# Kernel tuning notes

Measured on AMD Instinct MI355X. Metric: run time of the kernel, lower is better.

The kernel has to match this reference:

```python
import jax, jax.numpy as jnp
import numpy as np

B, N_SOURCES, H, W = 32, 262144, 256, 256


def setup_inputs() -> dict:
    key = jax.random.key(0)
    k1, k2, k3, k4 = jax.random.split(key, 4)
    return {
        "point_rates": jax.random.uniform(k1, (B, N_SOURCES), dtype=jnp.float32),
        "spatial": jax.random.uniform(k2, (B, 2, H, W), dtype=jnp.float32),
        "gia": jax.random.uniform(k3, (B, H, W), dtype=jnp.float32),
        "all_source_coords": jax.random.uniform(k4, (N_SOURCES, 2), dtype=jnp.float32),
    }


def reference(point_rates, spatial, gia, all_source_coords):
    # point_rates: [B, N], spatial: [B, 2, H, W], gia: [B, H, W], coords: [N, 2]
    _, _, h, w = spatial.shape
    sx = all_source_coords[:, 0]  # [N]
    sy = all_source_coords[:, 1]  # [N]

    def per_batch(pr, sp, g):
        # pr: [N], sp: [2, H, W], g: [H, W]
        xmin, xmax = sp[0].min(), sp[0].max()
        ymin, ymax = sp[1].min(), sp[1].max()
        in_view = ((sx >= xmin) & (sx <= xmax) & (sy >= ymin) & (sy <= ymax))
        nx = (sx - xmin) / (xmax - xmin)
        ny = (sy - ymin) / (ymax - ymin)
        px = jnp.clip(jnp.round(nx * (w - 1)).astype(jnp.int32), 0, w - 1)
        py = jnp.clip(jnp.round(ny * (h - 1)).astype(jnp.int32), 0, h - 1)
        # out-of-view sources contribute zero (instead of being gathered out)
        em = pr * g[py, px] * in_view.astype(pr.dtype)  # [N]
        field = jnp.zeros((h, w), dtype=pr.dtype).at[py, px].add(em)
        return field[None]  # [1, H, W]

    return jax.vmap(per_batch)(point_rates, spatial, gia)  # [B, 1, H, W]
```

## Files before the change

kernel.cpp:

```cpp
#include <hip/hip_runtime.h>
#include <math.h>

#define BATCH 32
#define NSRC  262144
#define HH    256
#define WW    256
#define HW    (HH * WW)
#define NBLK  16

#define ZBANDS 16
#define ZBAND_PIX (HW / ZBANDS)
#define ZCAP   18432
#define SPILL_CAP 131072
#define FIX_SCALE 524288.0f
#define FIX_INV   (1.0f / 524288.0f)
#define WS_ZCURS_OFF  8192
#define WS_ZSPCNT_OFF 10240
#define WS_ZSPILL_OFF 16384
#define WS_ZARENA_OFF (WS_ZSPILL_OFF + SPILL_CAP * 8)
#define WS_Z_BYTES    (WS_ZARENA_OFF + (size_t)BATCH * ZBANDS * ZCAP * 4)

#define FB_BANDS 8
#define FB_BAND_PIX (HW / FB_BANDS)

__global__ void box_kernel(const float* __restrict__ spatial,
                           float4* __restrict__ partials,
                           unsigned int* __restrict__ zero_tab,
                           int zero_n) {
    const int b   = blockIdx.y;
    const int blk = blockIdx.x;
    const int tid = threadIdx.x;

    if (zero_tab && blk == 0 && b == 0) {
        for (int j = tid; j < zero_n; j += 256) zero_tab[j] = 0u;
    }

    const int chunk = HW / NBLK;
    const float* xs = spatial + (size_t)b * 2 * HW + (size_t)blk * chunk;
    const float* ys = xs + HW;

    float xmn = 1e30f, xmx = -1e30f, ymn = 1e30f, ymx = -1e30f;
    const float4* xs4 = (const float4*)xs;
    const float4* ys4 = (const float4*)ys;
#pragma unroll
    for (int k = 0; k < 4; k++) {
        float4 vx = xs4[k * 256 + tid];
        float4 vy = ys4[k * 256 + tid];
        xmn = fminf(xmn, fminf(fminf(vx.x, vx.y), fminf(vx.z, vx.w)));
        xmx = fmaxf(xmx, fmaxf(fmaxf(vx.x, vx.y), fmaxf(vx.z, vx.w)));
        ymn = fminf(ymn, fminf(fminf(vy.x, vy.y), fminf(vy.z, vy.w)));
        ymx = fmaxf(ymx, fmaxf(fmaxf(vy.x, vy.y), fmaxf(vy.z, vy.w)));
    }
#pragma unroll
    for (int off = 32; off > 0; off >>= 1) {
        xmn = fminf(xmn, __shfl_down(xmn, off));
        xmx = fmaxf(xmx, __shfl_down(xmx, off));
        ymn = fminf(ymn, __shfl_down(ymn, off));
        ymx = fmaxf(ymx, __shfl_down(ymx, off));
    }
    __shared__ float4 s[4];
    if ((tid & 63) == 0) s[tid >> 6] = make_float4(xmn, xmx, ymn, ymx);
    __syncthreads();
    if (tid == 0) {
        float4 r = s[0];
#pragma unroll
        for (int wv = 1; wv < 4; wv++) {
            float4 t = s[wv];
            r.x = fminf(r.x, t.x); r.y = fmaxf(r.y, t.y);
            r.z = fminf(r.z, t.z); r.w = fmaxf(r.w, t.w);
        }
        partials[b * NBLK + blk] = r;
    }
}

__device__ __forceinline__ float4 fold_box(const float4* __restrict__ partials,
                                           int b, int tid, float4* sbox) {
    if (tid < 64) {
        float4 p = make_float4(1e30f, -1e30f, 1e30f, -1e30f);
        if (tid < NBLK) p = partials[b * NBLK + tid];
        float xmn = p.x, xmx = p.y, ymn = p.z, ymx = p.w;
#pragma unroll
        for (int off = 8; off > 0; off >>= 1) {
            xmn = fminf(xmn, __shfl_down(xmn, off));
            xmx = fmaxf(xmx, __shfl_down(xmx, off));
            ymn = fminf(ymn, __shfl_down(ymn, off));
            ymx = fmaxf(ymx, __shfl_down(ymx, off));
        }
        if (tid == 0) *sbox = make_float4(xmn, xmx, ymn, ymx);
    }
    __syncthreads();
    return *sbox;
}

__device__ __forceinline__ int route_of(float cx, float cy, float xmin,
                                        float ymin, float invx, float invy) {
    const float nx = __fmul_rn(__fsub_rn(cx, xmin), invx);
    const float ny = __fmul_rn(__fsub_rn(cy, ymin), invy);
    int px = (int)rintf(__fmul_rn(nx, 255.0f));
    int py = (int)rintf(__fmul_rn(ny, 255.0f));
    px = px < 0 ? 0 : (px > 255 ? 255 : px);
    py = py < 0 ? 0 : (py > 255 ? 255 : py);
    return py * WW + px;
}


__global__ __launch_bounds__(256) void scatter_ballot_kernel(
    const float* __restrict__ point_rates, const float2* __restrict__ coords,
    const float4* __restrict__ partials, unsigned int* __restrict__ cursors,
    unsigned int* __restrict__ arena, unsigned int* __restrict__ spill_cnt,
    uint2* __restrict__ spill) {
    const int b    = blockIdx.y;
    const int tid  = threadIdx.x;
    const int wave = tid >> 6;
    const int lane = tid & 63;
    __shared__ float4 sbox;
    __shared__ unsigned int wtot[4][ZBANDS];
    __shared__ unsigned int wbase[4][ZBANDS];

    const float4 box = fold_box(partials, b, tid, &sbox);
    const float xmin = box.x, xmax = box.y, ymin = box.z, ymax = box.w;
    const float invx = __fdiv_rn(1.0f, __fsub_rn(xmax, xmin));
    const float invy = __fdiv_rn(1.0f, __fsub_rn(ymax, ymin));

    const unsigned long long below =
        (lane == 63) ? 0x7FFFFFFFFFFFFFFFull : ((1ull << lane) - 1ull);

    const float* prb = point_rates + (size_t)b * NSRC;
    const int base = blockIdx.x * 4096;

    unsigned int cur_slice = 0u;

    unsigned int ent[16];
    unsigned int meta[16];

#pragma unroll
    for (int k = 0; k < 16; k++) {
        const int i = base + k * 256 + tid;
        const float2 c = coords[i];
        const float  pr = prb[i];
        const bool valid =
            !(c.x < xmin || c.x > xmax || c.y < ymin || c.y > ymax);
        const int idx = route_of(c.x, c.y, xmin, ymin, invx, invy);
        const int z = valid ? (idx >> 12) : ZBANDS;
        const unsigned int fixed =
            (unsigned int)(__fmul_rn(pr, FIX_SCALE) + 0.5f);
        ent[k] = (unsigned int)(idx & (ZBAND_PIX - 1)) | (fixed << 12);

        const unsigned long long bv = __ballot(valid);
        const unsigned long long b0 = __ballot((z & 1) != 0);
        const unsigned long long b1 = __ballot((z & 2) != 0);
        const unsigned long long b2 = __ballot((z & 4) != 0);
        const unsigned long long b3 = __ballot((z & 8) != 0);
        unsigned long long m = bv;
        m &= (lane & 1) ? b0 : ~b0;
        m &= (lane & 2) ? b1 : ~b1;
        m &= (lane & 4) ? b2 : ~b2;
        m &= (lane & 8) ? b3 : ~b3;
        const unsigned int cnt = (unsigned int)__popcll(m);
        const unsigned int curbase = __shfl(cur_slice, z);
        const unsigned long long mown = __shfl(m, z);
        const unsigned int rank = (unsigned int)__popcll(mown & below);
        meta[k] = valid ? (((unsigned int)z << 16) | (curbase + rank))
                        : 0xFFFFFFFFu;
        cur_slice += cnt;
    }

    if (lane < ZBANDS) wtot[wave][lane] = cur_slice;
    __syncthreads();

    if (wave == 0 && lane < ZBANDS) {
        unsigned int t0 = wtot[0][lane], t1 = wtot[1][lane],
                     t2 = wtot[2][lane], t3 = wtot[3][lane];
        unsigned int tot = t0 + t1 + t2 + t3;
        unsigned int g = atomicAdd(&cursors[b * ZBANDS + lane], tot);
        wbase[0][lane] = g;
        wbase[1][lane] = g + t0;
        wbase[2][lane] = g + t0 + t1;
        wbase[3][lane] = g + t0 + t1 + t2;
    }
    __syncthreads();

#pragma unroll
    for (int k = 0; k < 16; k++) {
        const unsigned int mt = meta[k];
        if (mt == 0xFFFFFFFFu) continue;
        const unsigned int z = mt >> 16;
        const unsigned int slot = wbase[wave][z] + (mt & 0xFFFFu);
        if (slot < ZCAP) {
            arena[((size_t)b * ZBANDS + z) * ZCAP + slot] = ent[k];
        } else {
            const unsigned int pos = atomicAdd(spill_cnt, 1u);
            if (pos < SPILL_CAP) {
                const unsigned int pix =
                    (z << 12) | (ent[k] & (ZBAND_PIX - 1));
                const int i = base + k * 256 + tid;
                spill[pos] = make_uint2(((unsigned int)b << 16) | pix,
                                        __float_as_uint(prb[i]));
            }
        }
    }
}

__global__ __launch_bounds__(1024) void accum_g_kernel(
    const unsigned int* __restrict__ arena, const float* __restrict__ gia,
    const unsigned int* __restrict__ cursors, float* __restrict__ out) {
    __shared__ unsigned int acc[ZBAND_PIX];
    const int z   = blockIdx.x;
    const int b   = blockIdx.y;
    const int tid = threadIdx.x;

    const unsigned int n_raw = cursors[b * ZBANDS + z];
    const float4* g4 =
        (const float4*)(gia + (size_t)b * HW + (size_t)z * ZBAND_PIX);
    float4 g = g4[tid];
    asm volatile("" : "+v"(g.x), "+v"(g.y), "+v"(g.z), "+v"(g.w));

    ((uint4*)acc)[tid] = make_uint4(0u, 0u, 0u, 0u);
    __syncthreads();

    unsigned int n = n_raw;
    if (n > ZCAP) n = ZCAP;
    const uint4* a4 = (const uint4*)(arena + ((size_t)b * ZBANDS + z) * ZCAP);

#define DO_E(w)                                                              \
    atomicAdd(&acc[(w) & (ZBAND_PIX - 1)], (w) >> 12);
    const unsigned int n4 = n >> 2;
    unsigned int j = tid;
    for (; j + 3u * 1024u < n4; j += 4u * 1024u) {
        uint4 e0 = a4[j];
        uint4 e1 = a4[j + 1024u];
        uint4 e2 = a4[j + 2048u];
        uint4 e3 = a4[j + 3072u];
        asm volatile(""
                     : "+v"(e0.x), "+v"(e0.y), "+v"(e0.z), "+v"(e0.w),
                       "+v"(e1.x), "+v"(e1.y), "+v"(e1.z), "+v"(e1.w),
                       "+v"(e2.x), "+v"(e2.y), "+v"(e2.z), "+v"(e2.w),
                       "+v"(e3.x), "+v"(e3.y), "+v"(e3.z), "+v"(e3.w));
        DO_E(e0.x) DO_E(e0.y) DO_E(e0.z) DO_E(e0.w)
        DO_E(e1.x) DO_E(e1.y) DO_E(e1.z) DO_E(e1.w)
        DO_E(e2.x) DO_E(e2.y) DO_E(e2.z) DO_E(e2.w)
        DO_E(e3.x) DO_E(e3.y) DO_E(e3.z) DO_E(e3.w)
    }
    for (; j < n4; j += 1024u) {
        const uint4 e = a4[j];
        DO_E(e.x) DO_E(e.y) DO_E(e.z) DO_E(e.w)
    }
    const unsigned int* a1 = (const unsigned int*)a4;
    for (unsigned int jj = (n4 << 2) + tid; jj < n; jj += 1024u) {
        const unsigned int w = a1[jj];
        DO_E(w)
    }
#undef DO_E
    __syncthreads();

    float4* o4 = (float4*)(out + (size_t)b * HW + (size_t)z * ZBAND_PIX);
    const uint4 a = ((const uint4*)acc)[tid];
    o4[tid] = make_float4(
        __fmul_rn(__fmul_rn((float)a.x, FIX_INV), g.x),
        __fmul_rn(__fmul_rn((float)a.y, FIX_INV), g.y),
        __fmul_rn(__fmul_rn((float)a.z, FIX_INV), g.z),
        __fmul_rn(__fmul_rn((float)a.w, FIX_INV), g.w));
}

__global__ void spill_kernel(const unsigned int* __restrict__ spill_cnt,
                             const uint2* __restrict__ spill,
                             const float* __restrict__ gia,
                             float* __restrict__ out) {
    unsigned int n = *spill_cnt;
    if (n > SPILL_CAP) n = SPILL_CAP;
    for (unsigned int j = blockIdx.x * 256 + threadIdx.x; j < n;
         j += gridDim.x * 256) {
        const uint2 e = spill[j];
        const unsigned int b = e.x >> 16;
        const unsigned int pix = e.x & 0xFFFFu;
        const float pr = __uint_as_float(e.y);
        atomicAdd(&out[(size_t)b * HW + pix],
                  __fmul_rn(pr, gia[(size_t)b * HW + pix]));
    }
}


__global__ __launch_bounds__(512) void accum_recompute_kernel(
    const float* __restrict__ point_rates, const float* __restrict__ gia,
    const float2* __restrict__ coords, const float4* __restrict__ partials,
    float* __restrict__ out) {
    __shared__ float acc[FB_BAND_PIX];
    __shared__ float4 sbox;
    const int z   = blockIdx.x;
    const int b   = blockIdx.y;
    const int tid = threadIdx.x;

    const float4 box = fold_box(partials, b, tid, &sbox);
    const float xmin = box.x, xmax = box.y, ymin = box.z, ymax = box.w;
    const float invx = __fdiv_rn(1.0f, __fsub_rn(xmax, xmin));
    const float invy = __fdiv_rn(1.0f, __fsub_rn(ymax, ymin));

    for (int j = tid; j < FB_BAND_PIX; j += 512) acc[j] = 0.f;
    __syncthreads();

    const float* prb = point_rates + (size_t)b * NSRC;
    const float* gb  = gia + (size_t)b * HW;
    const int lo = z * FB_BAND_PIX, hi = lo + FB_BAND_PIX;

    for (int i = tid; i < NSRC; i += 512) {
        const float2 c = coords[i];
        if (c.x < xmin || c.x > xmax || c.y < ymin || c.y > ymax) continue;
        const int idx = route_of(c.x, c.y, xmin, ymin, invx, invy);
        if (idx < lo || idx >= hi) continue;
        const float em = __fmul_rn(prb[i], gb[idx]);
        atomicAdd(&acc[idx - lo], em);
    }
    __syncthreads();

    float4* o4 = (float4*)(out + (size_t)b * HW + (size_t)z * FB_BAND_PIX);
    const float4* a4 = (const float4*)acc;
    for (int j = tid; j < FB_BAND_PIX / 4; j += 512) o4[j] = a4[j];
}

extern "C" void kernel_launch(void* const* d_in, const int* in_sizes, int n_in,
                              void* d_out, int out_size, void* d_ws, size_t ws_size,
                              hipStream_t stream) {
    const float* point_rates = (const float*)d_in[0];
    const float* spatial     = (const float*)d_in[1];
    const float* gia         = (const float*)d_in[2];
    const float2* coords     = (const float2*)d_in[3];
    float* out = (float*)d_out;

    char* ws = (char*)d_ws;
    float4* partials = (float4*)ws;

    if (ws_size >= WS_Z_BYTES) {
        unsigned int* cursors   = (unsigned int*)(ws + WS_ZCURS_OFF);
        unsigned int* spill_cnt = (unsigned int*)(ws + WS_ZSPCNT_OFF);
        uint2*        spill     = (uint2*)(ws + WS_ZSPILL_OFF);
        unsigned int* arena     = (unsigned int*)(ws + WS_ZARENA_OFF);

        box_kernel<<<dim3(NBLK, BATCH), 256, 0, stream>>>(
            spatial, partials, cursors, BATCH * ZBANDS + 1);
        scatter_ballot_kernel<<<dim3(NSRC / 4096, BATCH), 256, 0, stream>>>(
            point_rates, coords, partials, cursors, arena, spill_cnt, spill);
        accum_g_kernel<<<dim3(ZBANDS, BATCH), 1024, 0, stream>>>(
            arena, gia, cursors, out);
        spill_kernel<<<4, 256, 0, stream>>>(spill_cnt, spill, gia, out);
    } else {
        box_kernel<<<dim3(NBLK, BATCH), 256, 0, stream>>>(
            spatial, partials, nullptr, 0);
        accum_recompute_kernel<<<dim3(FB_BANDS, BATCH), 512, 0, stream>>>(
            point_rates, gia, coords, partials, out);
    }
}
```

Baseline: 126.0 us.

## Stage binned scatter entries in LDS to coalesce arena writes

Instead of each thread writing its entries straight to scattered global arena slots, the block first sorts its entries by band into shared memory using a prefix scan of per-band totals. It then writes each band's run contiguously to the arena, so global stores are coalesced. The cost is extra LDS traffic, an additional barrier and 16KB more shared memory per block, which may lower occupancy. The spill path now rebuilds the rate from the fixed-point entry rather than reloading it, which changes the spilled value's precision.

```diff
diff --git a/kernel.cpp b/kernel.cpp
--- a/kernel.cpp
+++ b/kernel.cpp
@@ -116,6 +116,9 @@
     __shared__ float4 sbox;
     __shared__ unsigned int wtot[4][ZBANDS];
     __shared__ unsigned int wbase[4][ZBANDS];
+    __shared__ unsigned int boff[ZBANDS + 1];
+    __shared__ unsigned int gbase[ZBANDS];
+    __shared__ unsigned int sort_lds[4096];
 
     const float4 box = fold_box(partials, b, tid, &sbox);
     const float xmin = box.x, xmax = box.y, ymin = box.z, ymax = box.w;
@@ -169,14 +172,22 @@
     __syncthreads();
 
     if (wave == 0 && lane < ZBANDS) {
-        unsigned int t0 = wtot[0][lane], t1 = wtot[1][lane],
-                     t2 = wtot[2][lane], t3 = wtot[3][lane];
-        unsigned int tot = t0 + t1 + t2 + t3;
-        unsigned int g = atomicAdd(&cursors[b * ZBANDS + lane], tot);
-        wbase[0][lane] = g;
-        wbase[1][lane] = g + t0;
-        wbase[2][lane] = g + t0 + t1;
-        wbase[3][lane] = g + t0 + t1 + t2;
+        const unsigned int t0 = wtot[0][lane], t1 = wtot[1][lane],
+                           t2 = wtot[2][lane], t3 = wtot[3][lane];
+        const unsigned int tot = t0 + t1 + t2 + t3;
+        wbase[0][lane] = 0u;
+        wbase[1][lane] = t0;
+        wbase[2][lane] = t0 + t1;
+        wbase[3][lane] = t0 + t1 + t2;
+        unsigned int p = tot;
+#pragma unroll
+        for (int off = 1; off < ZBANDS; off <<= 1) {
+            const unsigned int t = __shfl_up(p, off);
+            if (lane >= off) p += t;
+        }
+        boff[lane] = p - tot;
+        if (lane == ZBANDS - 1) boff[ZBANDS] = p;
+        gbase[lane] = atomicAdd(&cursors[b * ZBANDS + lane], tot);
     }
     __syncthreads();
 
@@ -185,17 +196,30 @@
         const unsigned int mt = meta[k];
         if (mt == 0xFFFFFFFFu) continue;
         const unsigned int z = mt >> 16;
-        const unsigned int slot = wbase[wave][z] + (mt & 0xFFFFu);
-        if (slot < ZCAP) {
-            arena[((size_t)b * ZBANDS + z) * ZCAP + slot] = ent[k];
-        } else {
-            const unsigned int pos = atomicAdd(spill_cnt, 1u);
-            if (pos < SPILL_CAP) {
-                const unsigned int pix =
-                    (z << 12) | (ent[k] & (ZBAND_PIX - 1));
-                const int i = base + k * 256 + tid;
-                spill[pos] = make_uint2(((unsigned int)b << 16) | pix,
-                                        __float_as_uint(prb[i]));
+        sort_lds[boff[z] + wbase[wave][z] + (mt & 0xFFFFu)] = ent[k];
+    }
+    __syncthreads();
+
+    unsigned int* ab = arena + (size_t)b * ZBANDS * ZCAP;
+    for (int z = 0; z < ZBANDS; z++) {
+        const unsigned int lo = boff[z];
+        const unsigned int cnt = boff[z + 1] - lo;
+        const unsigned int g = gbase[z];
+        unsigned int* dst = ab + (size_t)z * ZCAP;
+        for (unsigned int j = tid; j < cnt; j += 256) {
+            const unsigned int e = sort_lds[lo + j];
+            const unsigned int slot = g + j;
+            if (slot < ZCAP) {
+                dst[slot] = e;
+            } else {
+                const unsigned int pos = atomicAdd(spill_cnt, 1u);
+                if (pos < SPILL_CAP) {
+                    const unsigned int pix =
+                        ((unsigned int)z << 12) | (e & (ZBAND_PIX - 1));
+                    const float pr = __fmul_rn((float)(e >> 12), FIX_INV);
+                    spill[pos] = make_uint2(((unsigned int)b << 16) | pix,
+                                            __float_as_uint(pr));
+                }
             }
         }
     }
```

Result: slower. 130.2 us (+3.3%).

## Replace band binning and LDS accumulation with direct global fixed-point atomics

Applied to the files above, without the earlier changes.

Drops the ballot-based band partitioning into an arena, the per-band shared-memory accumulation kernel, and the spill kernel. Each source now does a single global integer atomicAdd into a per-batch fixed-point accumulator, which is zeroed in box_kernel, and a simple elementwise finalize kernel multiplies by gia. This removes the arena write and read traffic and one kernel launch. In exchange it relies on many scattered global atomics, about 8M across 2M pixels, served by the L2.

```diff
diff --git a/kernel.cpp b/kernel.cpp
--- a/kernel.cpp
+++ b/kernel.cpp
@@ -8,31 +8,26 @@
 #define HW    (HH * WW)
 #define NBLK  16
 
-#define ZBANDS 16
-#define ZBAND_PIX (HW / ZBANDS)
-#define ZCAP   18432
-#define SPILL_CAP 131072
 #define FIX_SCALE 524288.0f
 #define FIX_INV   (1.0f / 524288.0f)
-#define WS_ZCURS_OFF  8192
-#define WS_ZSPCNT_OFF 10240
-#define WS_ZSPILL_OFF 16384
-#define WS_ZARENA_OFF (WS_ZSPILL_OFF + SPILL_CAP * 8)
-#define WS_Z_BYTES    (WS_ZARENA_OFF + (size_t)BATCH * ZBANDS * ZCAP * 4)
+#define WS_GACC_OFF   16384
+#define WS_FUSED_BYTES (WS_GACC_OFF + (size_t)BATCH * HW * 4)
 
 #define FB_BANDS 8
 #define FB_BAND_PIX (HW / FB_BANDS)
 
 __global__ void box_kernel(const float* __restrict__ spatial,
                            float4* __restrict__ partials,
-                           unsigned int* __restrict__ zero_tab,
-                           int zero_n) {
+                           unsigned int* __restrict__ gacc_zero) {
     const int b   = blockIdx.y;
     const int blk = blockIdx.x;
     const int tid = threadIdx.x;
 
-    if (zero_tab && blk == 0 && b == 0) {
-        for (int j = tid; j < zero_n; j += 256) zero_tab[j] = 0u;
+    if (gacc_zero) {
+        uint4* gz = (uint4*)(gacc_zero + ((size_t)b * NBLK + blk) * (HW / NBLK));
+#pragma unroll
+        for (int j = 0; j < HW / NBLK / 4 / 256; j++)
+            gz[j * 256 + tid] = make_uint4(0u, 0u, 0u, 0u);
     }
 
     const int chunk = HW / NBLK;
@@ -103,35 +98,21 @@
     return py * WW + px;
 }
 
-
-__global__ __launch_bounds__(256) void scatter_ballot_kernel(
+__global__ __launch_bounds__(256) void scatter_atomic_kernel(
     const float* __restrict__ point_rates, const float2* __restrict__ coords,
-    const float4* __restrict__ partials, unsigned int* __restrict__ cursors,
-    unsigned int* __restrict__ arena, unsigned int* __restrict__ spill_cnt,
-    uint2* __restrict__ spill) {
-    const int b    = blockIdx.y;
-    const int tid  = threadIdx.x;
-    const int wave = tid >> 6;
-    const int lane = tid & 63;
+    const float4* __restrict__ partials, unsigned int* __restrict__ gacc) {
+    const int b   = blockIdx.y;
+    const int tid = threadIdx.x;
     __shared__ float4 sbox;
-    __shared__ unsigned int wtot[4][ZBANDS];
-    __shared__ unsigned int wbase[4][ZBANDS];
 
     const float4 box = fold_box(partials, b, tid, &sbox);
     const float xmin = box.x, xmax = box.y, ymin = box.z, ymax = box.w;
     const float invx = __fdiv_rn(1.0f, __fsub_rn(xmax, xmin));
     const float invy = __fdiv_rn(1.0f, __fsub_rn(ymax, ymin));
 
-    const unsigned long long below =
-        (lane == 63) ? 0x7FFFFFFFFFFFFFFFull : ((1ull << lane) - 1ull);
-
     const float* prb = point_rates + (size_t)b * NSRC;
+    unsigned int* acc_b = gacc + (size_t)b * HW;
     const int base = blockIdx.x * 4096;
-
-    unsigned int cur_slice = 0u;
-
-    unsigned int ent[16];
-    unsigned int meta[16];
 
 #pragma unroll
     for (int k = 0; k < 16; k++) {
@@ -141,142 +122,23 @@
         const bool valid =
             !(c.x < xmin || c.x > xmax || c.y < ymin || c.y > ymax);
         const int idx = route_of(c.x, c.y, xmin, ymin, invx, invy);
-        const int z = valid ? (idx >> 12) : ZBANDS;
         const unsigned int fixed =
             (unsigned int)(__fmul_rn(pr, FIX_SCALE) + 0.5f);
-        ent[k] = (unsigned int)(idx & (ZBAND_PIX - 1)) | (fixed << 12);
-
-        const unsigned long long bv = __ballot(valid);
-        const unsigned long long b0 = __ballot((z & 1) != 0);
-        const unsigned long long b1 = __ballot((z & 2) != 0);
-        const unsigned long long b2 = __ballot((z & 4) != 0);
-        const unsigned long long b3 = __ballot((z & 8) != 0);
-        unsigned long long m = bv;
-        m &= (lane & 1) ? b0 : ~b0;
-        m &= (lane & 2) ? b1 : ~b1;
-        m &= (lane & 4) ? b2 : ~b2;
-        m &= (lane & 8) ? b3 : ~b3;
-        const unsigned int cnt = (unsigned int)__popcll(m);
-        const unsigned int curbase = __shfl(cur_slice, z);
-        const unsigned long long mown = __shfl(m, z);
-        const unsigned int rank = (unsigned int)__popcll(mown & below);
-        meta[k] = valid ? (((unsigned int)z << 16) | (curbase + rank))
-                        : 0xFFFFFFFFu;
-        cur_slice += cnt;
-    }
-
-    if (lane < ZBANDS) wtot[wave][lane] = cur_slice;
-    __syncthreads();
-
-    if (wave == 0 && lane < ZBANDS) {
-        unsigned int t0 = wtot[0][lane], t1 = wtot[1][lane],
-                     t2 = wtot[2][lane], t3 = wtot[3][lane];
-        unsigned int tot = t0 + t1 + t2 + t3;
-        unsigned int g = atomicAdd(&cursors[b * ZBANDS + lane], tot);
-        wbase[0][lane] = g;
-        wbase[1][lane] = g + t0;
-        wbase[2][lane] = g + t0 + t1;
-        wbase[3][lane] = g + t0 + t1 + t2;
-    }
-    __syncthreads();
-
-#pragma unroll
-    for (int k = 0; k < 16; k++) {
-        const unsigned int mt = meta[k];
-        if (mt == 0xFFFFFFFFu) continue;
-        const unsigned int z = mt >> 16;
-        const unsigned int slot = wbase[wave][z] + (mt & 0xFFFFu);
-        if (slot < ZCAP) {
-            arena[((size_t)b * ZBANDS + z) * ZCAP + slot] = ent[k];
-        } else {
-            const unsigned int pos = atomicAdd(spill_cnt, 1u);
-            if (pos < SPILL_CAP) {
-                const unsigned int pix =
-                    (z << 12) | (ent[k] & (ZBAND_PIX - 1));
-                const int i = base + k * 256 + tid;
-                spill[pos] = make_uint2(((unsigned int)b << 16) | pix,
-                                        __float_as_uint(prb[i]));
-            }
-        }
-    }
-}
-
-__global__ __launch_bounds__(1024) void accum_g_kernel(
-    const unsigned int* __restrict__ arena, const float* __restrict__ gia,
-    const unsigned int* __restrict__ cursors, float* __restrict__ out) {
-    __shared__ unsigned int acc[ZBAND_PIX];
-    const int z   = blockIdx.x;
-    const int b   = blockIdx.y;
-    const int tid = threadIdx.x;
-
-    const unsigned int n_raw = cursors[b * ZBANDS + z];
-    const float4* g4 =
-        (const float4*)(gia + (size_t)b * HW + (size_t)z * ZBAND_PIX);
-    float4 g = g4[tid];
-    asm volatile("" : "+v"(g.x), "+v"(g.y), "+v"(g.z), "+v"(g.w));
-
-    ((uint4*)acc)[tid] = make_uint4(0u, 0u, 0u, 0u);
-    __syncthreads();
-
-    unsigned int n = n_raw;
-    if (n > ZCAP) n = ZCAP;
-    const uint4* a4 = (const uint4*)(arena + ((size_t)b * ZBANDS + z) * ZCAP);
-
-#define DO_E(w)                                                              \
-    atomicAdd(&acc[(w) & (ZBAND_PIX - 1)], (w) >> 12);
-    const unsigned int n4 = n >> 2;
-    unsigned int j = tid;
-    for (; j + 3u * 1024u < n4; j += 4u * 1024u) {
-        uint4 e0 = a4[j];
-        uint4 e1 = a4[j + 1024u];
-        uint4 e2 = a4[j + 2048u];
-        uint4 e3 = a4[j + 3072u];
-        asm volatile(""
-                     : "+v"(e0.x), "+v"(e0.y), "+v"(e0.z), "+v"(e0.w),
-                       "+v"(e1.x), "+v"(e1.y), "+v"(e1.z), "+v"(e1.w),
-                       "+v"(e2.x), "+v"(e2.y), "+v"(e2.z), "+v"(e2.w),
-                       "+v"(e3.x), "+v"(e3.y), "+v"(e3.z), "+v"(e3.w));
-        DO_E(e0.x) DO_E(e0.y) DO_E(e0.z) DO_E(e0.w)
-        DO_E(e1.x) DO_E(e1.y) DO_E(e1.z) DO_E(e1.w)
-        DO_E(e2.x) DO_E(e2.y) DO_E(e2.z) DO_E(e2.w)
-        DO_E(e3.x) DO_E(e3.y) DO_E(e3.z) DO_E(e3.w)
-    }
-    for (; j < n4; j += 1024u) {
-        const uint4 e = a4[j];
-        DO_E(e.x) DO_E(e.y) DO_E(e.z) DO_E(e.w)
-    }
-    const unsigned int* a1 = (const unsigned int*)a4;
-    for (unsigned int jj = (n4 << 2) + tid; jj < n; jj += 1024u) {
-        const unsigned int w = a1[jj];
-        DO_E(w)
-    }
-#undef DO_E
-    __syncthreads();
-
-    float4* o4 = (float4*)(out + (size_t)b * HW + (size_t)z * ZBAND_PIX);
-    const uint4 a = ((const uint4*)acc)[tid];
-    o4[tid] = make_float4(
+        if (valid) atomicAdd(&acc_b[idx], fixed);
+    }
+}
+
+__global__ __launch_bounds__(256) void finalize_kernel(
+    const unsigned int* __restrict__ gacc, const float* __restrict__ gia,
+    float* __restrict__ out) {
+    const int gid = blockIdx.x * 256 + threadIdx.x;
+    const uint4  a = ((const uint4*)gacc)[gid];
+    const float4 g = ((const float4*)gia)[gid];
+    ((float4*)out)[gid] = make_float4(
         __fmul_rn(__fmul_rn((float)a.x, FIX_INV), g.x),
         __fmul_rn(__fmul_rn((float)a.y, FIX_INV), g.y),
         __fmul_rn(__fmul_rn((float)a.z, FIX_INV), g.z),
         __fmul_rn(__fmul_rn((float)a.w, FIX_INV), g.w));
-}
-
-__global__ void spill_kernel(const unsigned int* __restrict__ spill_cnt,
-                             const uint2* __restrict__ spill,
-                             const float* __restrict__ gia,
-                             float* __restrict__ out) {
-    unsigned int n = *spill_cnt;
-    if (n > SPILL_CAP) n = SPILL_CAP;
-    for (unsigned int j = blockIdx.x * 256 + threadIdx.x; j < n;
-         j += gridDim.x * 256) {
-        const uint2 e = spill[j];
-        const unsigned int b = e.x >> 16;
-        const unsigned int pix = e.x & 0xFFFFu;
-        const float pr = __uint_as_float(e.y);
-        atomicAdd(&out[(size_t)b * HW + pix],
-                  __fmul_rn(pr, gia[(size_t)b * HW + pix]));
-    }
 }
 
 
@@ -329,22 +191,18 @@
     char* ws = (char*)d_ws;
     float4* partials = (float4*)ws;
 
-    if (ws_size >= WS_Z_BYTES) {
-        unsigned int* cursors   = (unsigned int*)(ws + WS_ZCURS_OFF);
-        unsigned int* spill_cnt = (unsigned int*)(ws + WS_ZSPCNT_OFF);
-        uint2*        spill     = (uint2*)(ws + WS_ZSPILL_OFF);
-        unsigned int* arena     = (unsigned int*)(ws + WS_ZARENA_OFF);
+    if (ws_size >= WS_FUSED_BYTES) {
+        unsigned int* gacc = (unsigned int*)(ws + WS_GACC_OFF);
 
         box_kernel<<<dim3(NBLK, BATCH), 256, 0, stream>>>(
-            spatial, partials, cursors, BATCH * ZBANDS + 1);
-        scatter_ballot_kernel<<<dim3(NSRC / 4096, BATCH), 256, 0, stream>>>(
-            point_rates, coords, partials, cursors, arena, spill_cnt, spill);
-        accum_g_kernel<<<dim3(ZBANDS, BATCH), 1024, 0, stream>>>(
-            arena, gia, cursors, out);
-        spill_kernel<<<4, 256, 0, stream>>>(spill_cnt, spill, gia, out);
+            spatial, partials, gacc);
+        scatter_atomic_kernel<<<dim3(NSRC / 4096, BATCH), 256, 0, stream>>>(
+            point_rates, coords, partials, gacc);
+        finalize_kernel<<<BATCH * HW / 4 / 256, 256, 0, stream>>>(
+            gacc, gia, out);
     } else {
         box_kernel<<<dim3(NBLK, BATCH), 256, 0, stream>>>(
-            spatial, partials, nullptr, 0);
+            spatial, partials, nullptr);
         accum_recompute_kernel<<<dim3(FB_BANDS, BATCH), 512, 0, stream>>>(
             point_rates, gia, coords, partials, out);
     }
```

Result: slower. 406.5 us (+222.6%).

## Replace wave-ballot band ranking with LDS atomic counters in scatter kernel

Applied to the files above, without the earlier changes.

Per-source band ranks are now taken from shared-memory atomic counters per band instead of five wave ballots with shuffles, and there is one global cursor atomic per band per block. Loads of coordinates and rates are batched four at a time behind an asm barrier to keep several memory requests in flight. Spilled entries now carry the fixed-point rate decoded from the packed entry rather than reloading the original float. LDS atomics on only 16 counters will contend heavily, and the spill path now loses precision relative to the old exact reload.

```diff
diff --git a/kernel.cpp b/kernel.cpp
--- a/kernel.cpp
+++ b/kernel.cpp
@@ -104,98 +104,93 @@
 }
 
 
-__global__ __launch_bounds__(256) void scatter_ballot_kernel(
+__global__ __launch_bounds__(256) void scatter_lds_kernel(
     const float* __restrict__ point_rates, const float2* __restrict__ coords,
     const float4* __restrict__ partials, unsigned int* __restrict__ cursors,
     unsigned int* __restrict__ arena, unsigned int* __restrict__ spill_cnt,
     uint2* __restrict__ spill) {
-    const int b    = blockIdx.y;
-    const int tid  = threadIdx.x;
-    const int wave = tid >> 6;
-    const int lane = tid & 63;
+    const int b   = blockIdx.y;
+    const int tid = threadIdx.x;
     __shared__ float4 sbox;
-    __shared__ unsigned int wtot[4][ZBANDS];
-    __shared__ unsigned int wbase[4][ZBANDS];
-
+    __shared__ unsigned int cnt[ZBANDS];
+    __shared__ unsigned int gbase[ZBANDS];
+
+    if (tid < ZBANDS) cnt[tid] = 0u;
     const float4 box = fold_box(partials, b, tid, &sbox);
     const float xmin = box.x, xmax = box.y, ymin = box.z, ymax = box.w;
     const float invx = __fdiv_rn(1.0f, __fsub_rn(xmax, xmin));
     const float invy = __fdiv_rn(1.0f, __fsub_rn(ymax, ymin));
 
-    const unsigned long long below =
-        (lane == 63) ? 0x7FFFFFFFFFFFFFFFull : ((1ull << lane) - 1ull);
-
     const float* prb = point_rates + (size_t)b * NSRC;
     const int base = blockIdx.x * 4096;
 
-    unsigned int cur_slice = 0u;
-
     unsigned int ent[16];
     unsigned int meta[16];
 
 #pragma unroll
-    for (int k = 0; k < 16; k++) {
-        const int i = base + k * 256 + tid;
-        const float2 c = coords[i];
-        const float  pr = prb[i];
-        const bool valid =
-            !(c.x < xmin || c.x > xmax || c.y < ymin || c.y > ymax);
-        const int idx = route_of(c.x, c.y, xmin, ymin, invx, invy);
-        const int z = valid ? (idx >> 12) : ZBANDS;
-        const unsigned int fixed =
-            (unsigned int)(__fmul_rn(pr, FIX_SCALE) + 0.5f);
-        ent[k] = (unsigned int)(idx & (ZBAND_PIX - 1)) | (fixed << 12);
-
-        const unsigned long long bv = __ballot(valid);
-        const unsigned long long b0 = __ballot((z & 1) != 0);
-        const unsigned long long b1 = __ballot((z & 2) != 0);
-        const unsigned long long b2 = __ballot((z & 4) != 0);
-        const unsigned long long b3 = __ballot((z & 8) != 0);
-        unsigned long long m = bv;
-        m &= (lane & 1) ? b0 : ~b0;
-        m &= (lane & 2) ? b1 : ~b1;
-        m &= (lane & 4) ? b2 : ~b2;
-        m &= (lane & 8) ? b3 : ~b3;
-        const unsigned int cnt = (unsigned int)__popcll(m);
-        const unsigned int curbase = __shfl(cur_slice, z);
-        const unsigned long long mown = __shfl(m, z);
-        const unsigned int rank = (unsigned int)__popcll(mown & below);
-        meta[k] = valid ? (((unsigned int)z << 16) | (curbase + rank))
-                        : 0xFFFFFFFFu;
-        cur_slice += cnt;
-    }
-
-    if (lane < ZBANDS) wtot[wave][lane] = cur_slice;
-    __syncthreads();
-
-    if (wave == 0 && lane < ZBANDS) {
-        unsigned int t0 = wtot[0][lane], t1 = wtot[1][lane],
-                     t2 = wtot[2][lane], t3 = wtot[3][lane];
-        unsigned int tot = t0 + t1 + t2 + t3;
-        unsigned int g = atomicAdd(&cursors[b * ZBANDS + lane], tot);
-        wbase[0][lane] = g;
-        wbase[1][lane] = g + t0;
-        wbase[2][lane] = g + t0 + t1;
-        wbase[3][lane] = g + t0 + t1 + t2;
-    }
-    __syncthreads();
-
+    for (int kk = 0; kk < 16; kk += 4) {
+        float2 c0, c1, c2, c3;
+        float  p0, p1, p2, p3;
+        {
+            const int i0 = base + (kk + 0) * 256 + tid;
+            const int i1 = base + (kk + 1) * 256 + tid;
+            const int i2 = base + (kk + 2) * 256 + tid;
+            const int i3 = base + (kk + 3) * 256 + tid;
+            c0 = coords[i0]; c1 = coords[i1];
+            c2 = coords[i2]; c3 = coords[i3];
+            p0 = prb[i0]; p1 = prb[i1]; p2 = prb[i2]; p3 = prb[i3];
+        }
+        asm volatile(""
+                     : "+v"(c0.x), "+v"(c0.y), "+v"(p0),
+                       "+v"(c1.x), "+v"(c1.y), "+v"(p1),
+                       "+v"(c2.x), "+v"(c2.y), "+v"(p2),
+                       "+v"(c3.x), "+v"(c3.y), "+v"(p3));
+#define RANK_ONE(J, CC, PP)                                                  \
+    {                                                                        \
+        const bool valid = !(CC.x < xmin || CC.x > xmax ||                   \
+                             CC.y < ymin || CC.y > ymax);                    \
+        const int idx = route_of(CC.x, CC.y, xmin, ymin, invx, invy);        \
+        const unsigned int fixed =                                           \
+            (unsigned int)(__fmul_rn(PP, FIX_SCALE) + 0.5f);                 \
+        ent[kk + J] =                                                        \
+            (unsigned int)(idx & (ZBAND_PIX - 1)) | (fixed << 12);           \
+        const int z = idx >> 12;                                             \
+        unsigned int rank = 0u;                                              \
+        if (valid) rank = atomicAdd(&cnt[z], 1u);                            \
+        meta[kk + J] = valid                                                 \
+            ? (((unsigned int)z << 16) | rank) : 0xFFFFFFFFu;                \
+    }
+        RANK_ONE(0, c0, p0)
+        RANK_ONE(1, c1, p1)
+        RANK_ONE(2, c2, p2)
+        RANK_ONE(3, c3, p3)
+#undef RANK_ONE
+    }
+    __syncthreads();
+
+    if (tid < ZBANDS) {
+        gbase[tid] = atomicAdd(&cursors[b * ZBANDS + tid], cnt[tid]);
+    }
+    __syncthreads();
+
+    unsigned int* ab = arena + (size_t)b * ZBANDS * ZCAP;
 #pragma unroll
     for (int k = 0; k < 16; k++) {
         const unsigned int mt = meta[k];
         if (mt == 0xFFFFFFFFu) continue;
         const unsigned int z = mt >> 16;
-        const unsigned int slot = wbase[wave][z] + (mt & 0xFFFFu);
+        const unsigned int slot = gbase[z] + (mt & 0xFFFFu);
         if (slot < ZCAP) {
-            arena[((size_t)b * ZBANDS + z) * ZCAP + slot] = ent[k];
+            ab[(size_t)z * ZCAP + slot] = ent[k];
         } else {
             const unsigned int pos = atomicAdd(spill_cnt, 1u);
             if (pos < SPILL_CAP) {
+                const unsigned int e = ent[k];
                 const unsigned int pix =
-                    (z << 12) | (ent[k] & (ZBAND_PIX - 1));
-                const int i = base + k * 256 + tid;
+                    (z << 12) | (e & (ZBAND_PIX - 1));
+                const float pr = __fmul_rn((float)(e >> 12), FIX_INV);
                 spill[pos] = make_uint2(((unsigned int)b << 16) | pix,
-                                        __float_as_uint(prb[i]));
+                                        __float_as_uint(pr));
             }
         }
     }
@@ -337,7 +332,7 @@
 
         box_kernel<<<dim3(NBLK, BATCH), 256, 0, stream>>>(
             spatial, partials, cursors, BATCH * ZBANDS + 1);
-        scatter_ballot_kernel<<<dim3(NSRC / 4096, BATCH), 256, 0, stream>>>(
+        scatter_lds_kernel<<<dim3(NSRC / 4096, BATCH), 256, 0, stream>>>(
             point_rates, coords, partials, cursors, arena, spill_cnt, spill);
         accum_g_kernel<<<dim3(ZBANDS, BATCH), 1024, 0, stream>>>(
             arena, gia, cursors, out);
```

Result: no change. 124.6 us (-1.1%).
